# Kernel tuning notes

Hardware: AMD Instinct MI355X
Metric: run time of the kernel (lower is better)

## Reference

```python
import jax, jax.numpy as jnp
import numpy as np

S = (128, 128, 128)  # spatial grid
K = (16, 16, 16)     # retained low-frequency modes


def _gelu(x):
    # torch nn.GELU default = exact erf variant
    return jax.nn.gelu(x, approximate=False)


def _flayer(x, Rr, Ri, w):
    # x: (s1,s2,s3,dv). Full rfftn then truncate to low modes (as in source).
    f = jnp.fft.rfftn(x, axes=(0, 1, 2))[: K[0], : K[1], : K[2]]  # (k1,k2,k3,dv) complex
    Rf = jnp.einsum('abcd,abcde->abce', f, Rr + 1j * Ri)           # per-mode channel mix
    kernelpart = jnp.fft.irfftn(Rf, s=S, axes=(0, 1, 2))           # zero-pad modes, back to grid
    return _gelu(kernelpart + x @ w)


def setup_inputs() -> dict:
    key = jax.random.key(0)
    ks = jax.random.split(key, 20)
    da, dv, dout = 4, 32, 1
    sc1, sc2, sc3 = 2.0 / da, 2.0 / dv, 2.0 / dv
    d = {}
    d['x'] = jax.random.normal(ks[0], (*S, da), dtype=jnp.float32)
    d['win'] = sc1 * jax.random.normal(ks[1], (da, dv), dtype=jnp.float32)
    d['bin1'] = sc1 * jax.random.normal(ks[2], (dv,), dtype=jnp.float32)
    i = 3
    for L in range(1, 5):
        d[f'Rphir{L}'] = sc2 * jax.random.normal(ks[i], (*K, dv, dv), dtype=jnp.float32); i += 1
        d[f'Rphii{L}'] = sc2 * jax.random.normal(ks[i], (*K, dv, dv), dtype=jnp.float32); i += 1
        d[f'w{L}'] = sc2 * jax.random.normal(ks[i], (dv, dv), dtype=jnp.float32); i += 1
    d['wout'] = sc3 * jax.random.normal(ks[i], (dv, dout), dtype=jnp.float32); i += 1
    d['bout'] = sc3 * jax.random.normal(ks[i], (dout,), dtype=jnp.float32)
    return d


def reference(x, win, bin1, Rphir1, Rphii1, w1, Rphir2, Rphii2, w2,
              Rphir3, Rphii3, w3, Rphir4, Rphii4, w4, wout, bout):
    v = _gelu(x @ win + bin1)          # lifting: (s1,s2,s3,dv)
    v = _flayer(v, Rphir1, Rphii1, w1)
    v = _flayer(v, Rphir2, Rphii2, w2)
    v = _flayer(v, Rphir3, Rphii3, w3)
    v = _flayer(v, Rphir4, Rphii4, w4)
    return v @ wout + bout             # (s1,s2,s3,dout)
```

## Files before the change

kernel.cpp:

```cpp
#include <hip/hip_runtime.h>
#include <math.h>

typedef float2 cplx;
typedef _Float16 h16;
typedef h16 h16x8 __attribute__((ext_vector_type(8)));
typedef float f32x4 __attribute__((ext_vector_type(4)));
typedef uint u32x2 __attribute__((ext_vector_type(2)));

#define MFMA16(a, b, c) __builtin_amdgcn_mfma_f32_16x16x32_f16(a, b, c, 0, 0, 0)

static __device__ __forceinline__ float gelu_exact(float z) {
  float x = z * 0.70710678118654752440f;
  float ax = fabsf(x);
  float t = __builtin_amdgcn_rcpf(fmaf(0.3275911f, ax, 1.0f));
  float p = fmaf(1.061405429f, t, -1.453152027f);
  p = fmaf(p, t, 1.421413741f);
  p = fmaf(p, t, -0.284496736f);
  p = fmaf(p, t, 0.254829592f);
  p = p * t;
  float e = __expf(-ax * ax);
  float erfax = fmaf(-p, e, 1.0f);
  float er = copysignf(erfax, x);
  return 0.5f * z * (1.0f + er);
}

template <int OFF>
static __device__ __forceinline__ h16x8 tr_frag(uint addr) {
  union { uint u[4]; h16x8 h; } r;
  u32x2 lo, hi;
  asm volatile("ds_read_b64_tr_b16 %0, %2 offset:%3\n\t"
               "ds_read_b64_tr_b16 %1, %2 offset:%4"
               : "=&v"(lo), "=&v"(hi)
               : "v"(addr), "i"(OFF), "i"(OFF + 128));
  r.u[0] = lo.x; r.u[1] = lo.y; r.u[2] = hi.x; r.u[3] = hi.y;
  return r.h;
}

__global__ __launch_bounds__(256) void k_prep(
    h16* __restrict__ Afwd, h16* __restrict__ Adt, cplx* __restrict__ Twc,
    const float* __restrict__ wA, const float* __restrict__ wB,
    const float* __restrict__ wC, const float* __restrict__ wD,
    h16* __restrict__ Wfr)
{
  const int tid = threadIdx.x;
  const float w0 = 0.049087385212340519f;
  for (int idx = tid; idx < 4096; idx += 256) {
    int Mt = idx >> 11, rem = idx & 2047, lane = rem >> 5, k = rem & 31;
    int j = k & 7, chunk = k >> 3;
    int m = lane & 15;
    int x3 = chunk * 32 + (lane >> 4) * 8 + j;
    float ang = (float)((m * x3) & 127) * w0;
    float s, c; sincosf(ang, &s, &c);
    float val = Mt ? s : c;
    h16 hi = (h16)val;
    Afwd[idx] = hi;
    Afwd[idx + 4096] = (h16)(val - (float)hi);
  }
  for (int idx = tid; idx < 4096; idx += 256) {
    int tt = idx >> 4, rem = idx & 15, t = rem >> 3, j = rem & 7;
    int wv = tt >> 6, lane = tt & 63, mrow = lane & 15, q = lane >> 4;
    int x3 = (2 * wv + t) * 16 + mrow;
    int kk = q * 8 + j;
    int m = (kk < 16) ? kk : kk - 16;
    float ang = (float)((x3 * m) & 127) * w0;
    float s, c; sincosf(ang, &s, &c);
    Adt[idx] = (h16)((kk < 16) ? c : s);
  }
  const float* ws[4] = { wA, wB, wC, wD };
  for (int idx = tid; idx < 16384; idx += 256) {
    int L = idx >> 12, rem = idx & 4095;
    int t2 = rem >> 4, nt = (rem >> 3) & 1, j = rem & 7;
    int mrow = t2 & 15, q = (t2 >> 4) & 3;
    int n = nt * 16 + mrow, kk = q * 8 + j;
    Wfr[idx] = (h16)ws[L][kk * 32 + n];
  }
  if (tid < 128) {
    float ang = (float)tid * w0;
    float s, c; sincosf(ang, &s, &c);
    Twc[tid] = make_float2(c, s);
  }
}

__global__ __launch_bounds__(256) void k_lift(
    const float* __restrict__ x, const float* __restrict__ win,
    const float* __restrict__ bin, h16* __restrict__ v)
{
  __shared__ float xr[512];
  __shared__ float wl[128];
  __shared__ float bl[32];
  const int tid = threadIdx.x;
  const size_t b = blockIdx.x;
  const float* xrow = x + b * 512;
  for (int i = tid; i < 512; i += 256) xr[i] = xrow[i];
  if (tid < 128) wl[tid] = win[tid];
  if (tid < 32)  bl[tid] = bin[tid];
  __syncthreads();
  const int c = tid & 31, g = tid >> 5;
  #pragma unroll
  for (int j = 0; j < 16; ++j) {
    int x3 = g + 8 * j;
    float z = bl[c];
    #pragma unroll
    for (int a = 0; a < 4; ++a) z += xr[x3 * 4 + a] * wl[a * 32 + c];
    v[b * 4096 + x3 * 32 + c] = (h16)gelu_exact(z);
  }
}

__global__ __launch_bounds__(256) void k_fwd3(
    const h16* __restrict__ v, const h16* __restrict__ Afwd, cplx* __restrict__ Gp,
    const cplx* __restrict__ twg)
{
  __shared__ __align__(16) h16 vtile[4][2][4][32][16];
  __shared__ cplx F3L[4][512];
  const int tid = threadIdx.x;
  const int x1 = blockIdx.x, qs = blockIdx.y;
  const int lane = tid & 63, wv = tid >> 6;
  const int mrow = lane & 15, q4 = lane >> 4;
  h16x8 Ah[2][4], Al[2][4];
  #pragma unroll
  for (int Mt = 0; Mt < 2; ++Mt)
    #pragma unroll
    for (int ch = 0; ch < 4; ++ch) {
      Ah[Mt][ch] = *(const h16x8*)&Afwd[Mt * 2048 + lane * 32 + ch * 8];
      Al[Mt][ch] = *(const h16x8*)&Afwd[4096 + Mt * 2048 + lane * 32 + ch * 8];
    }
  const uint ldsbase = (uint)(uintptr_t)&vtile[0][0][0][0][0];
  const uint abase = ldsbase + (uint)(wv * 8192 + q4 * 256 + mrow * 2);
  cplx g0[16], g1[16];
  #pragma unroll
  for (int k2 = 0; k2 < 16; ++k2) { g0[k2] = make_float2(0.f, 0.f); g1[k2] = make_float2(0.f, 0.f); }
  for (int it = 0; it < 8; ++it) {
    const int x2b = qs * 32 + it * 4;
    __syncthreads();
    const uint4* vsrc = (const uint4*)(v + ((size_t)x1 * 128 + x2b) * 4096);
    for (int i = tid; i < 2048; i += 256) {
      uint4 pk = vsrc[i];
      int rr = i >> 9, e = (i & 511) * 8, x3 = e >> 5, c0 = e & 31;
      int panel = c0 >> 4, off = c0 & 15;
      int chunk = x3 >> 5, row = x3 & 31;
      *(uint4*)&vtile[rr][panel][chunk][row][off] = pk;
    }
    __syncthreads();
    h16x8 B0[4], B1[4];
    {
      const uint a0 = abase;
      const uint a1 = abase + 4096;
      B0[0] = tr_frag<0>(a0);    B0[1] = tr_frag<1024>(a0);
      B0[2] = tr_frag<2048>(a0); B0[3] = tr_frag<3072>(a0);
      B1[0] = tr_frag<0>(a1);    B1[1] = tr_frag<1024>(a1);
      B1[2] = tr_frag<2048>(a1); B1[3] = tr_frag<3072>(a1);
      asm volatile("s_waitcnt lgkmcnt(0)" ::: "memory");
      __builtin_amdgcn_sched_barrier(0);
    }
    f32x4 acc[2][2];
    #pragma unroll
    for (int Mt = 0; Mt < 2; ++Mt)
      #pragma unroll
      for (int Nt = 0; Nt < 2; ++Nt) acc[Mt][Nt] = (f32x4){0.f, 0.f, 0.f, 0.f};
    #pragma unroll
    for (int ch = 0; ch < 4; ++ch) {
      acc[0][0] = MFMA16(Ah[0][ch], B0[ch], acc[0][0]);
      acc[0][0] = MFMA16(Al[0][ch], B0[ch], acc[0][0]);
      acc[0][1] = MFMA16(Ah[0][ch], B1[ch], acc[0][1]);
      acc[0][1] = MFMA16(Al[0][ch], B1[ch], acc[0][1]);
      acc[1][0] = MFMA16(Ah[1][ch], B0[ch], acc[1][0]);
      acc[1][0] = MFMA16(Al[1][ch], B0[ch], acc[1][0]);
      acc[1][1] = MFMA16(Ah[1][ch], B1[ch], acc[1][1]);
      acc[1][1] = MFMA16(Al[1][ch], B1[ch], acc[1][1]);
    }
    #pragma unroll
    for (int Nt = 0; Nt < 2; ++Nt)
      #pragma unroll
      for (int r = 0; r < 4; ++r)
        F3L[wv][(q4 * 4 + r) * 32 + Nt * 16 + mrow] =
            make_float2(acc[0][Nt][r], -acc[1][Nt][r]);
    __syncthreads();
    #pragma unroll
    for (int rr = 0; rr < 4; ++rr) {
      const int x2 = x2b + rr;
      cplx f0 = F3L[rr][tid], f1 = F3L[rr][tid + 256];
      #pragma unroll
      for (int k2 = 0; k2 < 16; ++k2) {
        cplx t = twg[(k2 * x2) & 127];
        g0[k2].x += f0.x * t.x + f0.y * t.y;  g0[k2].y += f0.y * t.x - f0.x * t.y;
        g1[k2].x += f1.x * t.x + f1.y * t.y;  g1[k2].y += f1.y * t.x - f1.x * t.y;
      }
    }
  }
  cplx* dst = Gp + (size_t)qs * 1048576;
  #pragma unroll
  for (int k2 = 0; k2 < 16; ++k2) {
    size_t base = ((size_t)x1 * 16 + k2) * 512;
    dst[base + tid] = g0[k2];
    dst[base + 256 + tid] = g1[k2];
  }
}

__global__ __launch_bounds__(512) void k_spec2(
    const cplx* __restrict__ Gp, const float* __restrict__ Rr,
    const float* __restrict__ Ri, cplx* __restrict__ H1,
    const cplx* __restrict__ twg)
{
  __shared__ cplx twc[128];
  __shared__ cplx fbp[2][512];
  __shared__ cplx tb[512];
  const int tid = threadIdx.x;
  const int k2 = blockIdx.x >> 4, k3 = blockIdx.x & 15;
  if (tid < 128) twc[tid] = twg[tid];
  __syncthreads();
  const int c = tid & 31, g = (tid >> 5) & 7, h = tid >> 8;
  float fr0 = 0.f, fi0 = 0.f, fr1 = 0.f, fi1 = 0.f;
  #pragma unroll 4
  for (int x1i = 0; x1i < 64; ++x1i) {
    const int x1 = h * 64 + x1i;
    size_t idx = (((size_t)x1 * 16 + k2) * 16 + k3) * 32 + c;
    cplx p0 = Gp[idx], p1 = Gp[idx + 1048576], p2 = Gp[idx + 2097152], p3 = Gp[idx + 3145728];
    cplx hh = make_float2(p0.x + p1.x + p2.x + p3.x, p0.y + p1.y + p2.y + p3.y);
    cplx ta = twc[(g * x1) & 127];
    cplx tb2 = twc[((g + 8) * x1) & 127];
    fr0 += hh.x * ta.x + hh.y * ta.y;   fi0 += hh.y * ta.x - hh.x * ta.y;
    fr1 += hh.x * tb2.x + hh.y * tb2.y; fi1 += hh.y * tb2.x - hh.x * tb2.y;
  }
  fbp[h][g * 32 + c] = make_float2(fr0, fi0);
  fbp[h][(g + 8) * 32 + c] = make_float2(fr1, fi1);
  __syncthreads();
  {
    cplx a = fbp[0][tid], b = fbp[1][tid];
    fbp[0][tid] = make_float2(a.x + b.x, a.y + b.y);
  }
  __syncthreads();
  {
    const int k1 = tid >> 5, e = c;
    float tr = 0.f, ti = 0.f;
    const size_t mb = ((size_t)k1 * 256 + k2 * 16 + k3) * 1024;
    #pragma unroll 4
    for (int cc = 0; cc < 32; ++cc) {
      float rr0 = Rr[mb + cc * 32 + e], ri0 = Ri[mb + cc * 32 + e];
      cplx f0 = fbp[0][k1 * 32 + cc];
      tr += f0.x * rr0 - f0.y * ri0;  ti += f0.x * ri0 + f0.y * rr0;
    }
    const float s = 4.76837158203125e-07f;
    tb[k1 * 32 + e] = make_float2(tr * s, ti * s);
  }
  __syncthreads();
  float trr[16], tii[16];
  #pragma unroll
  for (int k1 = 0; k1 < 16; ++k1) { cplx t = tb[k1 * 32 + c]; trr[k1] = t.x; tii[k1] = t.y; }
  #pragma unroll
  for (int jj = 0; jj < 8; ++jj) {
    int xx1 = g + 64 * h + 8 * jj;
    float hr = 0.f, hi = 0.f;
    #pragma unroll
    for (int k1 = 0; k1 < 16; ++k1) {
      cplx t = twc[(k1 * xx1) & 127];
      hr += trr[k1] * t.x - tii[k1] * t.y;
      hi += trr[k1] * t.y + tii[k1] * t.x;
    }
    H1[(((size_t)xx1 * 16 + k2) * 16 + k3) * 32 + c] = make_float2(hr, hi);
  }
}

__global__ __launch_bounds__(512) void k_ptm4(
    const cplx* __restrict__ H1, const h16* __restrict__ Wfr,
    h16* __restrict__ v, const h16* __restrict__ Adt,
    const cplx* __restrict__ twg)
{
  __shared__ __align__(16) h16 St[8][32 * 40];
  const int tid = threadIdx.x;
  const int x1 = blockIdx.y;
  const int x2b = blockIdx.x * 8;
  const int c = tid & 31, g2 = (tid >> 5) & 15;
  const int lane = tid & 63, w = tid >> 6;
  const int mrow = lane & 15, q = lane >> 4;
  h16x8 Adf, Bw[2];
  Adf   = *(const h16x8*)&Adt[((w >> 1) * 64 + lane) * 16 + (w & 1) * 8];
  Bw[0] = *(const h16x8*)&Wfr[lane * 16];
  Bw[1] = *(const h16x8*)&Wfr[lane * 16 + 8];
  cplx h1[16];
  {
    const cplx* h1p = H1 + (size_t)x1 * 8192;
    #pragma unroll
    for (int k2 = 0; k2 < 16; ++k2) h1[k2] = h1p[(k2 * 16 + g2) * 32 + c];
  }
  const float s0 = (g2 == 0) ? 1.f : 2.f;
  #pragma unroll
  for (int xi = 0; xi < 8; ++xi) {
    const int x2 = x2b + xi;
    float r = 0.f, i = 0.f;
    #pragma unroll
    for (int k2 = 0; k2 < 16; ++k2) {
      cplx t = twg[(k2 * x2) & 127];
      r += h1[k2].x * t.x - h1[k2].y * t.y;
      i += h1[k2].x * t.y + h1[k2].y * t.x;
    }
    St[xi][c * 40 + g2]      = (h16)(s0 * r);
    St[xi][c * 40 + 16 + g2] = (h16)(-s0 * i);
  }
  __syncthreads();
  for (int xi = 0; xi < 8; ++xi) {
    const size_t b = (size_t)x1 * 128 + x2b + xi;
    h16x8 Av = *(const h16x8*)&v[b * 4096 + (w * 16 + mrow) * 32 + q * 8];
    f32x4 acc[2];
    #pragma unroll
    for (int nt = 0; nt < 2; ++nt) {
      h16x8 Bst = *(const h16x8*)&St[xi][(nt * 16 + mrow) * 40 + q * 8];
      f32x4 z = {0.f, 0.f, 0.f, 0.f};
      z = MFMA16(Adf, Bst, z);
      z = MFMA16(Av, Bw[nt], z);
      acc[nt] = z;
    }
    #pragma unroll
    for (int nt = 0; nt < 2; ++nt)
      #pragma unroll
      for (int r2 = 0; r2 < 4; ++r2) {
        int x3 = w * 16 + q * 4 + r2;
        v[b * 4096 + x3 * 32 + nt * 16 + mrow] = (h16)gelu_exact(acc[nt][r2]);
      }
  }
}

__global__ __launch_bounds__(512) void k_ptf4(
    const cplx* __restrict__ H1, const h16* __restrict__ Wfr,
    const h16* __restrict__ v, const h16* __restrict__ Adt,
    const float* __restrict__ wout, const float* __restrict__ bout,
    float* __restrict__ out, const cplx* __restrict__ twg)
{
  __shared__ __align__(16) h16 St[8][32 * 40];
  const int tid = threadIdx.x;
  const int x1 = blockIdx.y;
  const int x2b = blockIdx.x * 8;
  const int c = tid & 31, g2 = (tid >> 5) & 15;
  const int lane = tid & 63, w = tid >> 6;
  const int mrow = lane & 15, q = lane >> 4;
  h16x8 Adf, Bw[2];
  Adf   = *(const h16x8*)&Adt[((w >> 1) * 64 + lane) * 16 + (w & 1) * 8];
  Bw[0] = *(const h16x8*)&Wfr[lane * 16];
  Bw[1] = *(const h16x8*)&Wfr[lane * 16 + 8];
  const float wo0 = wout[mrow], wo1 = wout[16 + mrow];
  const float bo = bout[0];
  cplx h1[16];
  {
    const cplx* h1p = H1 + (size_t)x1 * 8192;
    #pragma unroll
    for (int k2 = 0; k2 < 16; ++k2) h1[k2] = h1p[(k2 * 16 + g2) * 32 + c];
  }
  const float s0 = (g2 == 0) ? 1.f : 2.f;
  #pragma unroll
  for (int xi = 0; xi < 8; ++xi) {
    const int x2 = x2b + xi;
    float r = 0.f, i = 0.f;
    #pragma unroll
    for (int k2 = 0; k2 < 16; ++k2) {
      cplx t = twg[(k2 * x2) & 127];
      r += h1[k2].x * t.x - h1[k2].y * t.y;
      i += h1[k2].x * t.y + h1[k2].y * t.x;
    }
    St[xi][c * 40 + g2]      = (h16)(s0 * r);
    St[xi][c * 40 + 16 + g2] = (h16)(-s0 * i);
  }
  __syncthreads();
  for (int xi = 0; xi < 8; ++xi) {
    const size_t b = (size_t)x1 * 128 + x2b + xi;
    h16x8 Av = *(const h16x8*)&v[b * 4096 + (w * 16 + mrow) * 32 + q * 8];
    f32x4 acc[2];
    #pragma unroll
    for (int nt = 0; nt < 2; ++nt) {
      h16x8 Bst = *(const h16x8*)&St[xi][(nt * 16 + mrow) * 40 + q * 8];
      f32x4 z = {0.f, 0.f, 0.f, 0.f};
      z = MFMA16(Adf, Bst, z);
      z = MFMA16(Av, Bw[nt], z);
      acc[nt] = z;
    }
    #pragma unroll
    for (int r2 = 0; r2 < 4; ++r2) {
      float p = (float)(h16)gelu_exact(acc[0][r2]) * wo0
              + (float)(h16)gelu_exact(acc[1][r2]) * wo1;
      p += __shfl_xor(p, 1);
      p += __shfl_xor(p, 2);
      p += __shfl_xor(p, 4);
      p += __shfl_xor(p, 8);
      if (mrow == 0) {
        int x3 = w * 16 + q * 4 + r2;
        out[b * 128 + x3] = bo + p;
      }
    }
  }
}

__global__ void k_diag(float* out, float wsmb) {
  if (threadIdx.x == 0 && blockIdx.x == 0) out[0] = wsmb;
}

extern "C" void kernel_launch(void* const* d_in, const int* in_sizes, int n_in,
                              void* d_out, int out_size, void* d_ws, size_t ws_size,
                              hipStream_t stream)
{
  (void)in_sizes; (void)n_in; (void)out_size;
  const float* x    = (const float*)d_in[0];
  const float* win  = (const float*)d_in[1];
  const float* bin1 = (const float*)d_in[2];
  const float* Rr[4] = { (const float*)d_in[3], (const float*)d_in[6],
                         (const float*)d_in[9], (const float*)d_in[12] };
  const float* Ri[4] = { (const float*)d_in[4], (const float*)d_in[7],
                         (const float*)d_in[10], (const float*)d_in[13] };
  const float* wm[4] = { (const float*)d_in[5], (const float*)d_in[8],
                         (const float*)d_in[11], (const float*)d_in[14] };
  const float* wout = (const float*)d_in[15];
  const float* bout = (const float*)d_in[16];
  float* out = (float*)d_out;

  const size_t SZ_V  = 134217728;
  const size_t SZ_C  = 33554432;
  const size_t SZ_AF = 16384;
  const size_t SZ_AD = 8192;
  const size_t SZ_TW = 1024;
  const size_t SZ_WF = 32768;
  const size_t NEED = SZ_V + SZ_C + SZ_AF + SZ_AD + SZ_TW + SZ_WF;

  if (ws_size < NEED) {
    k_diag<<<1, 64, 0, stream>>>(out, (float)(ws_size >> 20));
    return;
  }
  char* p = (char*)d_ws;
  h16* v    = (h16*)p;  p += SZ_V;
  cplx* C   = (cplx*)p; p += SZ_C;
  h16* Afwd = (h16*)p;  p += SZ_AF;
  h16* Adt  = (h16*)p;  p += SZ_AD;
  cplx* Twc = (cplx*)p; p += SZ_TW;
  h16* Wfr  = (h16*)p;

  k_prep<<<1, 256, 0, stream>>>(Afwd, Adt, Twc, wm[0], wm[1], wm[2], wm[3], Wfr);
  k_lift<<<16384, 256, 0, stream>>>(x, win, bin1, v);
  for (int L = 0; L < 4; ++L) {
    k_fwd3<<<dim3(128, 4), 256, 0, stream>>>(v, Afwd, C, Twc);
    k_spec2<<<256, 512, 0, stream>>>(C, Rr[L], Ri[L], C, Twc);
    if (L < 3) k_ptm4<<<dim3(16, 128), 512, 0, stream>>>(C, Wfr + (size_t)L * 4096, v, Adt, Twc);
    else       k_ptf4<<<dim3(16, 128), 512, 0, stream>>>(C, Wfr + 3 * 4096, v, Adt, wout, bout, out, Twc);
  }
}
```

Measured before the change: 763.9 us.

## Split fwd3 k2 range across grid z and widen spectral kernel to 1024 threads

k_fwd3 gains a grid z dimension of 2, so each block accumulates only 8 of the 16 k2 twiddle outputs. This halves the accumulator registers and doubles the block count. The price is that each block repeats the v tile load and the MFMA x3 transform. The A fragments are now reloaded from global memory inside the loop instead of being held in registers, and a launch-bounds occupancy hint is added. The spectral kernel moves from 512 to 1024 threads, splitting the x1 reduction and the inverse k1 transform four ways to expose more parallelism per block.

```diff
diff --git a/kernel.cpp b/kernel.cpp
--- a/kernel.cpp
+++ b/kernel.cpp
@@ -106,29 +106,21 @@
   }
 }
 
-__global__ __launch_bounds__(256) void k_fwd3(
+__global__ __launch_bounds__(256, 4) void k_fwd3(
     const h16* __restrict__ v, const h16* __restrict__ Afwd, cplx* __restrict__ Gp,
     const cplx* __restrict__ twg)
 {
   __shared__ __align__(16) h16 vtile[4][2][4][32][16];
   __shared__ cplx F3L[4][512];
   const int tid = threadIdx.x;
-  const int x1 = blockIdx.x, qs = blockIdx.y;
+  const int x1 = blockIdx.x, qs = blockIdx.y, z = blockIdx.z;
   const int lane = tid & 63, wv = tid >> 6;
   const int mrow = lane & 15, q4 = lane >> 4;
-  h16x8 Ah[2][4], Al[2][4];
-  #pragma unroll
-  for (int Mt = 0; Mt < 2; ++Mt)
-    #pragma unroll
-    for (int ch = 0; ch < 4; ++ch) {
-      Ah[Mt][ch] = *(const h16x8*)&Afwd[Mt * 2048 + lane * 32 + ch * 8];
-      Al[Mt][ch] = *(const h16x8*)&Afwd[4096 + Mt * 2048 + lane * 32 + ch * 8];
-    }
   const uint ldsbase = (uint)(uintptr_t)&vtile[0][0][0][0][0];
   const uint abase = ldsbase + (uint)(wv * 8192 + q4 * 256 + mrow * 2);
-  cplx g0[16], g1[16];
-  #pragma unroll
-  for (int k2 = 0; k2 < 16; ++k2) { g0[k2] = make_float2(0.f, 0.f); g1[k2] = make_float2(0.f, 0.f); }
+  cplx g0[8], g1[8];
+  #pragma unroll
+  for (int k2 = 0; k2 < 8; ++k2) { g0[k2] = make_float2(0.f, 0.f); g1[k2] = make_float2(0.f, 0.f); }
   for (int it = 0; it < 8; ++it) {
     const int x2b = qs * 32 + it * 4;
     __syncthreads();
@@ -159,14 +151,18 @@
       for (int Nt = 0; Nt < 2; ++Nt) acc[Mt][Nt] = (f32x4){0.f, 0.f, 0.f, 0.f};
     #pragma unroll
     for (int ch = 0; ch < 4; ++ch) {
-      acc[0][0] = MFMA16(Ah[0][ch], B0[ch], acc[0][0]);
-      acc[0][0] = MFMA16(Al[0][ch], B0[ch], acc[0][0]);
-      acc[0][1] = MFMA16(Ah[0][ch], B1[ch], acc[0][1]);
-      acc[0][1] = MFMA16(Al[0][ch], B1[ch], acc[0][1]);
-      acc[1][0] = MFMA16(Ah[1][ch], B0[ch], acc[1][0]);
-      acc[1][0] = MFMA16(Al[1][ch], B0[ch], acc[1][0]);
-      acc[1][1] = MFMA16(Ah[1][ch], B1[ch], acc[1][1]);
-      acc[1][1] = MFMA16(Al[1][ch], B1[ch], acc[1][1]);
+      h16x8 Ah0 = *(const h16x8*)&Afwd[lane * 32 + ch * 8];
+      h16x8 Al0 = *(const h16x8*)&Afwd[4096 + lane * 32 + ch * 8];
+      h16x8 Ah1 = *(const h16x8*)&Afwd[2048 + lane * 32 + ch * 8];
+      h16x8 Al1 = *(const h16x8*)&Afwd[6144 + lane * 32 + ch * 8];
+      acc[0][0] = MFMA16(Ah0, B0[ch], acc[0][0]);
+      acc[0][0] = MFMA16(Al0, B0[ch], acc[0][0]);
+      acc[0][1] = MFMA16(Ah0, B1[ch], acc[0][1]);
+      acc[0][1] = MFMA16(Al0, B1[ch], acc[0][1]);
+      acc[1][0] = MFMA16(Ah1, B0[ch], acc[1][0]);
+      acc[1][0] = MFMA16(Al1, B0[ch], acc[1][0]);
+      acc[1][1] = MFMA16(Ah1, B1[ch], acc[1][1]);
+      acc[1][1] = MFMA16(Al1, B1[ch], acc[1][1]);
     }
     #pragma unroll
     for (int Nt = 0; Nt < 2; ++Nt)
@@ -180,8 +176,8 @@
       const int x2 = x2b + rr;
       cplx f0 = F3L[rr][tid], f1 = F3L[rr][tid + 256];
       #pragma unroll
-      for (int k2 = 0; k2 < 16; ++k2) {
-        cplx t = twg[(k2 * x2) & 127];
+      for (int k2 = 0; k2 < 8; ++k2) {
+        cplx t = twg[((z * 8 + k2) * x2) & 127];
         g0[k2].x += f0.x * t.x + f0.y * t.y;  g0[k2].y += f0.y * t.x - f0.x * t.y;
         g1[k2].x += f1.x * t.x + f1.y * t.y;  g1[k2].y += f1.y * t.x - f1.x * t.y;
       }
@@ -189,20 +185,20 @@
   }
   cplx* dst = Gp + (size_t)qs * 1048576;
   #pragma unroll
-  for (int k2 = 0; k2 < 16; ++k2) {
-    size_t base = ((size_t)x1 * 16 + k2) * 512;
+  for (int k2 = 0; k2 < 8; ++k2) {
+    size_t base = ((size_t)x1 * 16 + z * 8 + k2) * 512;
     dst[base + tid] = g0[k2];
     dst[base + 256 + tid] = g1[k2];
   }
 }
 
-__global__ __launch_bounds__(512) void k_spec2(
+__global__ __launch_bounds__(1024) void k_spec3(
     const cplx* __restrict__ Gp, const float* __restrict__ Rr,
     const float* __restrict__ Ri, cplx* __restrict__ H1,
     const cplx* __restrict__ twg)
 {
   __shared__ cplx twc[128];
-  __shared__ cplx fbp[2][512];
+  __shared__ cplx fbp[4][512];
   __shared__ cplx tb[512];
   const int tid = threadIdx.x;
   const int k2 = blockIdx.x >> 4, k3 = blockIdx.x & 15;
@@ -211,8 +207,8 @@
   const int c = tid & 31, g = (tid >> 5) & 7, h = tid >> 8;
   float fr0 = 0.f, fi0 = 0.f, fr1 = 0.f, fi1 = 0.f;
   #pragma unroll 4
-  for (int x1i = 0; x1i < 64; ++x1i) {
-    const int x1 = h * 64 + x1i;
+  for (int x1i = 0; x1i < 32; ++x1i) {
+    const int x1 = h * 32 + x1i;
     size_t idx = (((size_t)x1 * 16 + k2) * 16 + k3) * 32 + c;
     cplx p0 = Gp[idx], p1 = Gp[idx + 1048576], p2 = Gp[idx + 2097152], p3 = Gp[idx + 3145728];
     cplx hh = make_float2(p0.x + p1.x + p2.x + p3.x, p0.y + p1.y + p2.y + p3.y);
@@ -224,12 +220,12 @@
   fbp[h][g * 32 + c] = make_float2(fr0, fi0);
   fbp[h][(g + 8) * 32 + c] = make_float2(fr1, fi1);
   __syncthreads();
-  {
-    cplx a = fbp[0][tid], b = fbp[1][tid];
-    fbp[0][tid] = make_float2(a.x + b.x, a.y + b.y);
-  }
-  __syncthreads();
-  {
+  if (tid < 512) {
+    cplx a = fbp[0][tid], b = fbp[1][tid], d = fbp[2][tid], e = fbp[3][tid];
+    fbp[0][tid] = make_float2((a.x + b.x) + (d.x + e.x), (a.y + b.y) + (d.y + e.y));
+  }
+  __syncthreads();
+  if (tid < 512) {
     const int k1 = tid >> 5, e = c;
     float tr = 0.f, ti = 0.f;
     const size_t mb = ((size_t)k1 * 256 + k2 * 16 + k3) * 1024;
@@ -247,8 +243,8 @@
   #pragma unroll
   for (int k1 = 0; k1 < 16; ++k1) { cplx t = tb[k1 * 32 + c]; trr[k1] = t.x; tii[k1] = t.y; }
   #pragma unroll
-  for (int jj = 0; jj < 8; ++jj) {
-    int xx1 = g + 64 * h + 8 * jj;
+  for (int jj = 0; jj < 4; ++jj) {
+    int xx1 = g + 8 * (h * 4 + jj);
     float hr = 0.f, hi = 0.f;
     #pragma unroll
     for (int k1 = 0; k1 < 16; ++k1) {
@@ -432,8 +428,8 @@
   k_prep<<<1, 256, 0, stream>>>(Afwd, Adt, Twc, wm[0], wm[1], wm[2], wm[3], Wfr);
   k_lift<<<16384, 256, 0, stream>>>(x, win, bin1, v);
   for (int L = 0; L < 4; ++L) {
-    k_fwd3<<<dim3(128, 4), 256, 0, stream>>>(v, Afwd, C, Twc);
-    k_spec2<<<256, 512, 0, stream>>>(C, Rr[L], Ri[L], C, Twc);
+    k_fwd3<<<dim3(128, 4, 2), 256, 0, stream>>>(v, Afwd, C, Twc);
+    k_spec3<<<256, 1024, 0, stream>>>(C, Rr[L], Ri[L], C, Twc);
     if (L < 3) k_ptm4<<<dim3(16, 128), 512, 0, stream>>>(C, Wfr + (size_t)L * 4096, v, Adt, Twc);
     else       k_ptf4<<<dim3(16, 128), 512, 0, stream>>>(C, Wfr + 3 * 4096, v, Adt, wout, bout, out, Twc);
   }
```

Result: slower. 931.0 us (+21.9%).
